# Performance work log

Hardware: AMD Instinct MI355X
Metric: run time of the kernel (lower is better)

Reference implementation:

```python
import jax, jax.numpy as jnp
from jax import lax
import numpy as np

B = 2; Hs = 48; Ws = 48
DIM = 768; NH = 6; NP = 4; DH = DIM // NH; HID = int(DIM * 0.25)
LIN = Hs * Ws                    # feat tokens (single deform level)
LQ = 21 * (Hs * Ws) // 4         # query tokens: (2H*2W)+(H*W)+(H/2*W/2)


def _ln(x, g, b, eps=1e-6):
    m = jnp.mean(x, -1, keepdims=True)
    v = jnp.mean((x - m) ** 2, -1, keepdims=True)
    return (x - m) * lax.rsqrt(v + eps) * g + b


def _bilinear_sample(value, loc, Hf, Wf):
    """value: [B,NH,Hf*Wf,DH]; loc: [B,Lq,NH,NP,2] normalized to [0,1].
    Matches F.grid_sample(align_corners=False, padding_mode='zeros')."""
    Bq, nH = value.shape[0], value.shape[1]
    Lq = loc.shape[1]
    x = loc[..., 0] * Wf - 0.5
    y = loc[..., 1] * Hf - 0.5
    x0 = jnp.floor(x); y0 = jnp.floor(y)
    wx1 = x - x0; wy1 = y - y0
    x0i = x0.astype(jnp.int32); y0i = y0.astype(jnp.int32)

    def tr(a):  # [B,Lq,NH,NP] -> [B,NH,Lq*NP]
        return jnp.transpose(a, (0, 2, 1, 3)).reshape(Bq, nH, Lq * NP)

    def gather(yi, xi):
        valid = ((xi >= 0) & (xi < Wf) & (yi >= 0) & (yi < Hf)).astype(value.dtype)
        idx = jnp.clip(yi, 0, Hf - 1) * Wf + jnp.clip(xi, 0, Wf - 1)
        g = jnp.take_along_axis(value, tr(idx)[..., None], axis=2)  # [B,NH,Lq*NP,DH]
        return g * tr(valid)[..., None]

    out = (gather(y0i, x0i) * tr((1 - wy1) * (1 - wx1))[..., None]
         + gather(y0i, x0i + 1) * tr((1 - wy1) * wx1)[..., None]
         + gather(y0i + 1, x0i) * tr(wy1 * (1 - wx1))[..., None]
         + gather(y0i + 1, x0i + 1) * tr(wy1 * wx1)[..., None])
    return out.reshape(Bq, nH, Lq, NP, DH)


def _dwconv(x_tokens, w, b, h, w_):
    Bq, n_tok, C = x_tokens.shape
    img = jnp.transpose(x_tokens, (0, 2, 1)).reshape(Bq, C, h, w_)
    y = lax.conv_general_dilated(img, w, (1, 1), 'SAME',
                                 dimension_numbers=('NCHW', 'OIHW', 'NCHW'),
                                 feature_group_count=C) + b[None, :, None, None]
    return jnp.transpose(y.reshape(Bq, C, h * w_), (0, 2, 1))


def _forward(query, reference_points, feat, qn_g, qn_b, fn_g, fn_b, vW, vb,
             soW, sob, awW, awb, opW, opb, mn_g, mn_b,
             fc1W, fc1b, dwW, dwb, fc2W, fc2b, H, W):
    Bq, Lq, C = query.shape
    q = _ln(query, qn_g, qn_b)
    v = _ln(feat, fn_g, fn_b) @ vW + vb                             # [B,Lin,C]
    value = jnp.transpose(v.reshape(Bq, -1, NH, DH), (0, 2, 1, 3))  # [B,NH,Lin,DH]
    offs = (q @ soW + sob).reshape(Bq, Lq, NH, NP, 2)
    attw = jax.nn.softmax((q @ awW + awb).reshape(Bq, Lq, NH, NP), axis=-1)
    norm = jnp.asarray([W, H], dtype=q.dtype)                       # (x,y) normalizer
    loc = reference_points.reshape(Bq, Lq, 1, 1, 2) + offs / norm   # [B,Lq,NH,NP,2]
    samp = _bilinear_sample(value, loc, H, W)                       # [B,NH,Lq,NP,DH]
    aw = jnp.transpose(attw, (0, 2, 1, 3))[..., None]               # [B,NH,Lq,NP,1]
    out = jnp.sum(samp * aw, axis=3)                                # [B,NH,Lq,DH]
    out = jnp.transpose(out, (0, 2, 1, 3)).reshape(Bq, Lq, C) @ opW + opb
    x = query + out                                                 # residual
    # multi-scale conv MLP
    h = _ln(x, mn_g, mn_b) @ fc1W + fc1b                            # [B,Lq,HID]
    n = Lq // 21
    h = jnp.concatenate([
        _dwconv(h[:, :16 * n], dwW, dwb, 2 * H, 2 * W),
        _dwconv(h[:, 16 * n:20 * n], dwW, dwb, H, W),
        _dwconv(h[:, 20 * n:], dwW, dwb, H // 2, W // 2)], axis=1)
    h = jax.nn.gelu(h, approximate=False)
    h = h @ fc2W + fc2b
    return x + h


def setup_inputs():
    key = jax.random.key(0)
    ks = jax.random.split(key, 16)
    s = 0.02
    return dict(
        query=jax.random.normal(ks[0], (B, LQ, DIM), jnp.float32),
        reference_points=jax.random.uniform(ks[1], (B, LQ, 1, 2), jnp.float32),
        feat=jax.random.normal(ks[2], (B, LIN, DIM), jnp.float32),
        spatial_shapes=jnp.array([[Hs, Ws]], jnp.int32),
        level_start_index=jnp.array([0], jnp.int32),
        H=Hs, W=Ws,
        qn_g=jnp.ones((DIM,)), qn_b=jnp.zeros((DIM,)),
        fn_g=jnp.ones((DIM,)), fn_b=jnp.zeros((DIM,)),
        mn_g=jnp.ones((DIM,)), mn_b=jnp.zeros((DIM,)),
        vW=s * jax.random.normal(ks[3], (DIM, DIM)), vb=jnp.zeros((DIM,)),
        soW=s * jax.random.normal(ks[4], (DIM, NH * NP * 2)),
        sob=0.5 * jax.random.normal(ks[5], (NH * NP * 2,)),
        awW=s * jax.random.normal(ks[6], (DIM, NH * NP)), awb=jnp.zeros((NH * NP,)),
        opW=s * jax.random.normal(ks[7], (DIM, DIM)), opb=jnp.zeros((DIM,)),
        fc1W=s * jax.random.normal(ks[8], (DIM, HID)), fc1b=jnp.zeros((HID,)),
        dwW=s * jax.random.normal(ks[9], (HID, 1, 3, 3)), dwb=jnp.zeros((HID,)),
        fc2W=s * jax.random.normal(ks[10], (HID, DIM)), fc2b=jnp.zeros((DIM,)),
    )


def reference(query, reference_points, feat, spatial_shapes, level_start_index, H, W,
              qn_g, qn_b, fn_g, fn_b, mn_g, mn_b, vW, vb, soW, sob, awW, awb,
              opW, opb, fc1W, fc1b, dwW, dwb, fc2W, fc2b):
    del spatial_shapes, level_start_index  # single level; H,W are static ints
    return _forward(query, reference_points, feat, qn_g, qn_b, fn_g, fn_b, vW, vb,
                    soW, sob, awW, awb, opW, opb, mn_g, mn_b,
                    fc1W, fc1b, dwW, dwb, fc2W, fc2b, H, W)
```

## Files before the change

kernel.cpp:

```cpp
#include <hip/hip_runtime.h>

#define NB    2
#define LQT   12096
#define LINT  2304
#define DIMC  768
#define NHD   6
#define NPT   4
#define DHD   128
#define HIDC  192
#define HH    48
#define WW    48

typedef __attribute__((ext_vector_type(8))) short bf16x8;
typedef __attribute__((ext_vector_type(4))) float f32x4;
typedef __attribute__((ext_vector_type(8))) unsigned short u16x8;

__device__ __forceinline__ unsigned short f2bf(float f) {
  unsigned int u = __builtin_bit_cast(unsigned int, f);
  u += 0x7FFFu + ((u >> 16) & 1u);
  return (unsigned short)(u >> 16);
}

__device__ __forceinline__ void gload16(const unsigned short* g, unsigned short* l) {
  __builtin_amdgcn_global_load_lds(
      (const __attribute__((address_space(1))) unsigned int*)g,
      (__attribute__((address_space(3))) unsigned int*)l, 16, 0, 0);
}

__global__ __launch_bounds__(256) void pack_wt(const float* __restrict__ src,
                                               unsigned short* __restrict__ dst,
                                               int K, int N, int rows) {
  size_t i = (size_t)blockIdx.x * 256 + threadIdx.x;
  if (i >= (size_t)rows * K) return;
  int n = (int)(i / K), k = (int)(i % K);
  float v = (n < N) ? src[(size_t)k * N + n] : 0.f;
  dst[i] = f2bf(v);
}

__global__ __launch_bounds__(256) void pack_soaw(const float* __restrict__ soW,
                                                 const float* __restrict__ awW,
                                                 const float* __restrict__ sob,
                                                 const float* __restrict__ awb,
                                                 unsigned short* __restrict__ dst,
                                                 float* __restrict__ bdst) {
  size_t i = (size_t)blockIdx.x * 256 + threadIdx.x;
  if (i < 128) bdst[i] = (i < 48) ? sob[i] : (i < 72 ? awb[i - 48] : 0.f);
  if (i >= (size_t)128 * DIMC) return;
  int n = (int)(i / DIMC), k = (int)(i % DIMC);
  float v = (n < 48) ? soW[(size_t)k * 48 + n]
                     : (n < 72 ? awW[(size_t)k * 24 + (n - 48)] : 0.f);
  dst[i] = f2bf(v);
}

__global__ __launch_bounds__(256) void ln_to_bf16(const float* __restrict__ in,
                                                  const float* __restrict__ gamma,
                                                  const float* __restrict__ beta,
                                                  unsigned short* __restrict__ out) {
  const int row = blockIdx.x;
  const int t = threadIdx.x;
  const float* x = in + (size_t)row * DIMC;
  float v0 = x[t], v1 = x[t + 256], v2 = x[t + 512];
  float s = v0 + v1 + v2;
  float s2 = v0 * v0 + v1 * v1 + v2 * v2;
#pragma unroll
  for (int o = 32; o > 0; o >>= 1) {
    s += __shfl_down(s, o);
    s2 += __shfl_down(s2, o);
  }
  __shared__ float red[8];
  const int wave = t >> 6, lane = t & 63;
  if (lane == 0) { red[wave] = s; red[wave + 4] = s2; }
  __syncthreads();
  float S = red[0] + red[1] + red[2] + red[3];
  float S2 = red[4] + red[5] + red[6] + red[7];
  float mean = S * (1.0f / DIMC);
  float var = S2 * (1.0f / DIMC) - mean * mean;
  float inv = rsqrtf(var + 1e-6f);
  unsigned short* o0 = out + (size_t)row * DIMC;
  o0[t]       = f2bf((v0 - mean) * inv * gamma[t]       + beta[t]);
  o0[t + 256] = f2bf((v1 - mean) * inv * gamma[t + 256] + beta[t + 256]);
  o0[t + 512] = f2bf((v2 - mean) * inv * gamma[t + 512] + beta[t + 512]);
}

template <bool HAS_ADD>
__global__ __launch_bounds__(256) void gemm_bt(const unsigned short* __restrict__ A,
                                               const unsigned short* __restrict__ Bt,
                                               const float* __restrict__ bias,
                                               const float* __restrict__ add,
                                               float* __restrict__ out,
                                               int M, int N, int K) {
  __shared__ unsigned short As[128 * 64];
  __shared__ unsigned short Bs[128 * 64];
  const int t = threadIdx.x;
  const int wave = t >> 6, lane = t & 63;
  const int m0 = blockIdx.x * 128;
  const int n0 = blockIdx.y * 128;
  const int wm = (wave >> 1) * 64, wn = (wave & 1) * 64;
  const int lr = lane & 15;
  const int lg = lane >> 4;

  const int srow = wave * 32 + (lane >> 3);
  const int sslot = lane & 7;

  f32x4 acc[4][4] = {};

  for (int k0 = 0; k0 < K; k0 += 64) {
    __syncthreads();
#pragma unroll
    for (int i = 0; i < 4; ++i) {
      const int row = srow + i * 8;
      const int ca = sslot ^ (row & 7);
      gload16(A  + (size_t)(m0 + row) * K + k0 + ca * 8, As + (wave * 32 + i * 8) * 64);
      gload16(Bt + (size_t)(n0 + row) * K + k0 + ca * 8, Bs + (wave * 32 + i * 8) * 64);
    }
    __syncthreads();

    bf16x8 af[2][4], bg[2][4];
#pragma unroll
    for (int kk = 0; kk < 2; ++kk) {
#pragma unroll
      for (int i = 0; i < 4; ++i) {
        int row = wm + i * 16 + lr;
        int slot = (kk * 4 + lg) ^ (row & 7);
        af[kk][i] = *(const bf16x8*)(As + row * 64 + slot * 8);
        row = wn + i * 16 + lr;
        slot = (kk * 4 + lg) ^ (row & 7);
        bg[kk][i] = *(const bf16x8*)(Bs + row * 64 + slot * 8);
      }
    }
#pragma unroll
    for (int kk = 0; kk < 2; ++kk)
#pragma unroll
      for (int i = 0; i < 4; ++i)
#pragma unroll
        for (int j = 0; j < 4; ++j)
          acc[i][j] = __builtin_amdgcn_mfma_f32_16x16x32_bf16(af[kk][i], bg[kk][j], acc[i][j], 0, 0, 0);
  }

  const int orow = lg * 4;
#pragma unroll
  for (int i = 0; i < 4; ++i) {
#pragma unroll
    for (int j = 0; j < 4; ++j) {
      const int n = n0 + wn + j * 16 + lr;
      if (n < N) {
#pragma unroll
        for (int r = 0; r < 4; ++r) {
          const int m = m0 + wm + i * 16 + orow + r;
          float v = acc[i][j][r] + bias[n];
          if (HAS_ADD) v += add[(size_t)m * N + n];
          out[(size_t)m * N + n] = v;
        }
      }
    }
  }
}

__global__ __launch_bounds__(192) void deform_attn(const float* __restrict__ soaw,
                                                   const float* __restrict__ rp,
                                                   const float* __restrict__ value,
                                                   unsigned short* __restrict__ attn) {
  const int row = blockIdx.x;
  const int b = row / LQT;
  const int t = threadIdx.x;
  const int h = t >> 5;
  const int l = t & 31;
  const float* sa = soaw + (size_t)row * 128;
  const float bx = rp[(size_t)row * 2 + 0] * (float)WW - 0.5f;
  const float by = rp[(size_t)row * 2 + 1] * (float)HH - 0.5f;

  float lg0 = sa[48 + h * 4 + 0], lg1 = sa[48 + h * 4 + 1];
  float lg2 = sa[48 + h * 4 + 2], lg3 = sa[48 + h * 4 + 3];
  float mx = fmaxf(fmaxf(lg0, lg1), fmaxf(lg2, lg3));
  float e0 = expf(lg0 - mx), e1 = expf(lg1 - mx), e2 = expf(lg2 - mx), e3 = expf(lg3 - mx);
  float inv = 1.0f / (e0 + e1 + e2 + e3);
  float awp[4] = {e0 * inv, e1 * inv, e2 * inv, e3 * inv};

  const float* vb = value + (size_t)b * LINT * DIMC + h * DHD + l * 4;
  float ax = 0.f, ay = 0.f, az = 0.f, aw = 0.f;
#pragma unroll
  for (int p = 0; p < 4; ++p) {
    float fx = bx + sa[h * 8 + p * 2 + 0];
    float fy = by + sa[h * 8 + p * 2 + 1];
    float x0f = floorf(fx), y0f = floorf(fy);
    float wx = fx - x0f, wy = fy - y0f;
    int x0 = (int)x0f, y0 = (int)y0f;
#pragma unroll
    for (int dy = 0; dy < 2; ++dy) {
#pragma unroll
      for (int dx = 0; dx < 2; ++dx) {
        int xi = x0 + dx, yi = y0 + dy;
        float w = (dy ? wy : 1.f - wy) * (dx ? wx : 1.f - wx) * awp[p];
        if (xi < 0 || xi >= WW || yi < 0 || yi >= HH) w = 0.f;
        int xc = min(max(xi, 0), WW - 1), yc = min(max(yi, 0), HH - 1);
        const float4 g = *(const float4*)(vb + (size_t)(yc * WW + xc) * DIMC);
        ax += w * g.x; ay += w * g.y; az += w * g.z; aw += w * g.w;
      }
    }
  }
  unsigned short* op = attn + (size_t)row * DIMC + h * DHD + l * 4;
  ushort4 ov;
  ov.x = f2bf(ax); ov.y = f2bf(ay); ov.z = f2bf(az); ov.w = f2bf(aw);
  *(ushort4*)op = ov;
}

__global__ __launch_bounds__(192) void dwconv_gelu(const float* __restrict__ h1,
                                                   const float* __restrict__ dwW,
                                                   const float* __restrict__ dwb,
                                                   unsigned short* __restrict__ out) {
  const int blk = blockIdx.x;
  const int b = blk / LQT;
  const int q = blk % LQT;
  int base, Wi, Hi;
  if (q < 9216)       { base = 0;     Wi = 96; Hi = 96; }
  else if (q < 11520) { base = 9216;  Wi = 48; Hi = 48; }
  else                { base = 11520; Wi = 24; Hi = 24; }
  const int loc = q - base;
  const int y = loc / Wi, x = loc % Wi;
  const int c = threadIdx.x;
  const float* src = h1 + ((size_t)b * LQT + base) * HIDC + c;
  float acc = dwb[c];
#pragma unroll
  for (int dy = -1; dy <= 1; ++dy) {
    int yy = y + dy;
    if (yy < 0 || yy >= Hi) continue;
#pragma unroll
    for (int dx = -1; dx <= 1; ++dx) {
      int xx = x + dx;
      if (xx < 0 || xx >= Wi) continue;
      acc += dwW[c * 9 + (dy + 1) * 3 + (dx + 1)] * src[(size_t)(yy * Wi + xx) * HIDC];
    }
  }
  float g = 0.5f * acc * (1.0f + erff(acc * 0.70710678118654752f));
  out[(size_t)blk * HIDC + c] = f2bf(g);
}

extern "C" void kernel_launch(void* const* d_in, const int* in_sizes, int n_in,
                              void* d_out, int out_size, void* d_ws, size_t ws_size,
                              hipStream_t stream) {
  const float* query = (const float*)d_in[0];
  const float* rp    = (const float*)d_in[1];
  const float* feat  = (const float*)d_in[2];
  const float* qn_g  = (const float*)d_in[7];
  const float* qn_b  = (const float*)d_in[8];
  const float* fn_g  = (const float*)d_in[9];
  const float* fn_b  = (const float*)d_in[10];
  const float* mn_g  = (const float*)d_in[11];
  const float* mn_b  = (const float*)d_in[12];
  const float* vW    = (const float*)d_in[13];
  const float* vb    = (const float*)d_in[14];
  const float* soW   = (const float*)d_in[15];
  const float* sob   = (const float*)d_in[16];
  const float* awW   = (const float*)d_in[17];
  const float* awb   = (const float*)d_in[18];
  const float* opW   = (const float*)d_in[19];
  const float* opb   = (const float*)d_in[20];
  const float* fc1W  = (const float*)d_in[21];
  const float* fc1b  = (const float*)d_in[22];
  const float* dwW   = (const float*)d_in[23];
  const float* dwb   = (const float*)d_in[24];
  const float* fc2W  = (const float*)d_in[25];
  const float* fc2b  = (const float*)d_in[26];
  float* out = (float*)d_out;
  (void)in_sizes; (void)n_in; (void)out_size; (void)ws_size;

  char* ws = (char*)d_ws;
  size_t off = 0;
  auto alloc = [&](size_t bytes) -> void* {
    off = (off + 255) & ~(size_t)255;
    void* p = ws + off;
    off += bytes;
    return p;
  };

  const int MQ = NB * LQT;
  const int MF = NB * LINT;

  unsigned short* vWt    = (unsigned short*)alloc((size_t)768 * 768 * 2);
  unsigned short* opWt   = (unsigned short*)alloc((size_t)768 * 768 * 2);
  unsigned short* soawWt = (unsigned short*)alloc((size_t)128 * 768 * 2);
  unsigned short* fc1Wt  = (unsigned short*)alloc((size_t)256 * 768 * 2);
  unsigned short* fc2Wt  = (unsigned short*)alloc((size_t)768 * 192 * 2);
  float*          soawb  = (float*)alloc(128 * 4);
  unsigned short* f_ln   = (unsigned short*)alloc((size_t)MF * DIMC * 2);
  unsigned short* q_ln   = (unsigned short*)alloc((size_t)MQ * DIMC * 2);
  float*          value  = (float*)alloc((size_t)MF * DIMC * 4);
  float*          soaw   = (float*)alloc((size_t)MQ * 128 * 4);
  unsigned short* attnb  = (unsigned short*)alloc((size_t)MQ * DIMC * 2);
  float*          xbuf   = (float*)alloc((size_t)MQ * DIMC * 4);

  float* h1 = (float*)attnb;
  unsigned short* coutb = (unsigned short*)soaw;
  unsigned short* lnx = q_ln;

  pack_wt<<<dim3((768 * 768 + 255) / 256), dim3(256), 0, stream>>>(vW, vWt, 768, 768, 768);
  pack_wt<<<dim3((768 * 768 + 255) / 256), dim3(256), 0, stream>>>(opW, opWt, 768, 768, 768);
  pack_wt<<<dim3((256 * 768 + 255) / 256), dim3(256), 0, stream>>>(fc1W, fc1Wt, 768, 192, 256);
  pack_wt<<<dim3((768 * 192 + 255) / 256), dim3(256), 0, stream>>>(fc2W, fc2Wt, 192, 768, 768);
  pack_soaw<<<dim3((128 * 768 + 255) / 256), dim3(256), 0, stream>>>(soW, awW, sob, awb, soawWt, soawb);

  ln_to_bf16<<<dim3(MF), dim3(256), 0, stream>>>(feat, fn_g, fn_b, f_ln);
  ln_to_bf16<<<dim3(MQ), dim3(256), 0, stream>>>(query, qn_g, qn_b, q_ln);

  gemm_bt<false><<<dim3(MF / 128, 6), dim3(256), 0, stream>>>(f_ln, vWt, vb, nullptr, value, MF, 768, 768);

  gemm_bt<false><<<dim3(MQ / 128, 1), dim3(256), 0, stream>>>(q_ln, soawWt, soawb, nullptr, soaw, MQ, 128, 768);

  deform_attn<<<dim3(MQ), dim3(192), 0, stream>>>(soaw, rp, value, attnb);

  gemm_bt<true><<<dim3(MQ / 128, 6), dim3(256), 0, stream>>>(attnb, opWt, opb, query, xbuf, MQ, 768, 768);

  ln_to_bf16<<<dim3(MQ), dim3(256), 0, stream>>>(xbuf, mn_g, mn_b, lnx);

  gemm_bt<false><<<dim3(MQ / 128, 2), dim3(256), 0, stream>>>(lnx, fc1Wt, fc1b, nullptr, h1, MQ, 192, 768);

  dwconv_gelu<<<dim3(MQ), dim3(192), 0, stream>>>(h1, dwW, dwb, coutb);

  gemm_bt<true><<<dim3(MQ / 128, 6), dim3(256), 0, stream>>>(coutb, fc2Wt, fc2b, xbuf, out, MQ, 768, 192);
}
```

Before: 346.9 us.

## Double-buffer GEMM LDS tiles and remap blocks per XCD for L2 locality

```diff
diff --git a/kernel.cpp b/kernel.cpp
--- a/kernel.cpp
+++ b/kernel.cpp
@@ -88,13 +88,19 @@
                                                const float* __restrict__ bias,
                                                const float* __restrict__ add,
                                                float* __restrict__ out,
-                                               int M, int N, int K) {
-  __shared__ unsigned short As[128 * 64];
-  __shared__ unsigned short Bs[128 * 64];
+                                               int M, int N, int K, int nn) {
+  __shared__ unsigned short As[2][128 * 64];
+  __shared__ unsigned short Bs[2][128 * 64];
   const int t = threadIdx.x;
   const int wave = t >> 6, lane = t & 63;
-  const int m0 = blockIdx.x * 128;
-  const int n0 = blockIdx.y * 128;
+
+  const int nwg = gridDim.x;
+  const int qq = nwg >> 3, rr = nwg & 7;
+  const int xcd = blockIdx.x & 7, pos = blockIdx.x >> 3;
+  const int swz = ((xcd < rr) ? xcd * (qq + 1) : rr * (qq + 1) + (xcd - rr) * qq) + pos;
+  const int m0 = (swz / nn) * 128;
+  const int n0 = (swz % nn) * 128;
+
   const int wm = (wave >> 1) * 64, wn = (wave & 1) * 64;
   const int lr = lane & 15;
   const int lg = lane >> 4;
@@ -102,18 +108,24 @@
   const int srow = wave * 32 + (lane >> 3);
   const int sslot = lane & 7;
 
-  f32x4 acc[4][4] = {};
-
-  for (int k0 = 0; k0 < K; k0 += 64) {
-    __syncthreads();
+  auto stage = [&](int buf, int k0) {
 #pragma unroll
     for (int i = 0; i < 4; ++i) {
       const int row = srow + i * 8;
       const int ca = sslot ^ (row & 7);
-      gload16(A  + (size_t)(m0 + row) * K + k0 + ca * 8, As + (wave * 32 + i * 8) * 64);
-      gload16(Bt + (size_t)(n0 + row) * K + k0 + ca * 8, Bs + (wave * 32 + i * 8) * 64);
-    }
-    __syncthreads();
+      gload16(A  + (size_t)(m0 + row) * K + k0 + ca * 8, &As[buf][(wave * 32 + i * 8) * 64]);
+      gload16(Bt + (size_t)(n0 + row) * K + k0 + ca * 8, &Bs[buf][(wave * 32 + i * 8) * 64]);
+    }
+  };
+
+  f32x4 acc[4][4] = {};
+
+  stage(0, 0);
+  __syncthreads();
+  int cur = 0;
+
+  for (int k0 = 0; k0 < K; k0 += 64) {
+    if (k0 + 64 < K) stage(cur ^ 1, k0 + 64);
 
     bf16x8 af[2][4], bg[2][4];
 #pragma unroll
@@ -122,10 +134,10 @@
       for (int i = 0; i < 4; ++i) {
         int row = wm + i * 16 + lr;
         int slot = (kk * 4 + lg) ^ (row & 7);
-        af[kk][i] = *(const bf16x8*)(As + row * 64 + slot * 8);
+        af[kk][i] = *(const bf16x8*)(&As[cur][row * 64 + slot * 8]);
         row = wn + i * 16 + lr;
         slot = (kk * 4 + lg) ^ (row & 7);
-        bg[kk][i] = *(const bf16x8*)(Bs + row * 64 + slot * 8);
+        bg[kk][i] = *(const bf16x8*)(&Bs[cur][row * 64 + slot * 8]);
       }
     }
 #pragma unroll
@@ -135,6 +147,9 @@
 #pragma unroll
         for (int j = 0; j < 4; ++j)
           acc[i][j] = __builtin_amdgcn_mfma_f32_16x16x32_bf16(af[kk][i], bg[kk][j], acc[i][j], 0, 0, 0);
+
+    __syncthreads();
+    cur ^= 1;
   }
 
   const int orow = lg * 4;
@@ -302,19 +317,19 @@
   ln_to_bf16<<<dim3(MF), dim3(256), 0, stream>>>(feat, fn_g, fn_b, f_ln);
   ln_to_bf16<<<dim3(MQ), dim3(256), 0, stream>>>(query, qn_g, qn_b, q_ln);
 
-  gemm_bt<false><<<dim3(MF / 128, 6), dim3(256), 0, stream>>>(f_ln, vWt, vb, nullptr, value, MF, 768, 768);
-
-  gemm_bt<false><<<dim3(MQ / 128, 1), dim3(256), 0, stream>>>(q_ln, soawWt, soawb, nullptr, soaw, MQ, 128, 768);
+  gemm_bt<false><<<dim3((MF / 128) * 6), dim3(256), 0, stream>>>(f_ln, vWt, vb, nullptr, value, MF, 768, 768, 6);
+
+  gemm_bt<false><<<dim3(MQ / 128), dim3(256), 0, stream>>>(q_ln, soawWt, soawb, nullptr, soaw, MQ, 128, 768, 1);
 
   deform_attn<<<dim3(MQ), dim3(192), 0, stream>>>(soaw, rp, value, attnb);
 
-  gemm_bt<true><<<dim3(MQ / 128, 6), dim3(256), 0, stream>>>(attnb, opWt, opb, query, xbuf, MQ, 768, 768);
+  gemm_bt<true><<<dim3((MQ / 128) * 6), dim3(256), 0, stream>>>(attnb, opWt, opb, query, xbuf, MQ, 768, 768, 6);
 
   ln_to_bf16<<<dim3(MQ), dim3(256), 0, stream>>>(xbuf, mn_g, mn_b, lnx);
 
-  gemm_bt<false><<<dim3(MQ / 128, 2), dim3(256), 0, stream>>>(lnx, fc1Wt, fc1b, nullptr, h1, MQ, 192, 768);
+  gemm_bt<false><<<dim3((MQ / 128) * 2), dim3(256), 0, stream>>>(lnx, fc1Wt, fc1b, nullptr, h1, MQ, 192, 768, 2);
 
   dwconv_gelu<<<dim3(MQ), dim3(192), 0, stream>>>(h1, dwW, dwb, coutb);
 
-  gemm_bt<true><<<dim3(MQ / 128, 6), dim3(256), 0, stream>>>(coutb, fc2Wt, fc2b, xbuf, out, MQ, 768, 192);
-}
+  gemm_bt<true><<<dim3((MQ / 128) * 6), dim3(256), 0, stream>>>(coutb, fc2Wt, fc2b, xbuf, out, MQ, 768, 192, 6);
+}
```

New measurement: 336.1 us. -3.1%, faster.
